# Performance work log

Measured on AMD Instinct MI355X. Metric: run time of the kernel, lower is better.

The kernel has to match this reference:

```python
import jax, jax.numpy as jnp
import numpy as np

IC, OC, ID, OD = 1152, 10, 8, 16   # input_caps, output_caps, input_dim, output_dim
N_ITER = 5
THRESHOLD = 1e-05
EPS = 1e-20


def setup_inputs() -> dict:
    key = jax.random.key(0)
    k1, k2 = jax.random.split(key)
    x = jax.random.uniform(k1, (32, IC, ID), dtype=jnp.float32)
    # replicate CapsLayer.__init__ + norm_weights(): uniform(0,1), normalize over
    # output_caps dim, clamp to threshold, renormalize
    w = jax.random.uniform(k2, (IC, OC, ID, OD), dtype=jnp.float32)
    w = w / (w.sum(axis=1, keepdims=True) + EPS)
    w = jnp.clip(w, THRESHOLD, None)
    w = w / (w.sum(axis=1, keepdims=True) + EPS)
    return {"x": x, "weights": w}


def nnmf_sbs(inp, weights):
    # inp: [B, ic, id], weights: [ic, oc, id, od] -> out: [B, ic, oc, od]
    B = inp.shape[0]
    out0 = jnp.full((B, IC, OC, OD), 1.0 / OD, dtype=inp.dtype)

    def body(out, _):
        h_w = out[:, :, :, None, :] * weights[None]          # [B,ic,oc,id,od]
        h_w = h_w / (h_w.sum(-1, keepdims=True) + EPS)       # normalize over od
        h_w = (h_w * inp[:, :, None, :, None]).sum(-2)       # reduce id -> [B,ic,oc,od]
        out = h_w / (h_w.sum(-1, keepdims=True) + EPS)       # normalize over od
        return out, None

    out, _ = jax.lax.scan(body, out0, None, length=N_ITER)
    return out


def reference(x, weights):
    x = x / (x.sum(-1, keepdims=True) + EPS)                 # normalize over input_dim
    h = nnmf_sbs(x, weights)                                 # [B,ic,oc,od]
    # reconstruct = (h.unsqueeze(-2) * weights).sum(-1) -> [B,ic,oc,id]
    reconstruct = jnp.einsum('bicd,iced->bice', h, weights)
    alpha = jnp.einsum('bice,bie->bic', reconstruct, x)      # [B,ic,oc]
    alpha = alpha / (alpha.sum(-1, keepdims=True) + EPS)     # normalize over oc
    return jnp.einsum('bicd,bic->bcd', h, alpha)             # sum over ic -> [B,oc,od]
```

## Files before the change

### kernel.cpp

```cpp
#include <hip/hip_runtime.h>

#define B_   32
#define ICN  1152
#define OCN  10
#define IDN  8
#define ODN  16
#define ODH  8
#define NIT  5
#define EPS  1e-20f
#define OUTN (B_ * OCN * ODN)
#define BGRP 11
#define NWAVE (BGRP * ICN)
#define WPB  4
#define NBLK (NWAVE / WPB)

__device__ __forceinline__ float dpp_swap1(float x) {
  return __int_as_float(__builtin_amdgcn_update_dpp(
      0, __float_as_int(x), 0xB1, 0xF, 0xF, true));
}

__global__ __launch_bounds__(256, 4) void caps_main(
    const float* __restrict__ xg, const float* __restrict__ wg,
    float* __restrict__ ws, float* __restrict__ outg, int atomic_out) {
  const int l = threadIdx.x & 63;
  const int wid = blockIdx.x * WPB + (threadIdx.x >> 6);
  const int ic = wid % ICN;
  const int bgrp = wid / ICN;
  const int grp = l / 20;
  const int q = l % 20;
  const int oc = q >> 1;
  const int half = q & 1;
  const int b = bgrp * 3 + grp;
  const bool valid = (grp < 3) && (b < B_);
  const int bb = (b < B_) ? b : (B_ - 1);

  float wr[IDN][ODH];
  {
    const float* wp = wg + ((size_t)ic * OCN + oc) * (IDN * ODN) + half * ODH;
#pragma unroll
    for (int id = 0; id < IDN; ++id) {
      const float4 v0 = *(const float4*)(wp + id * ODN);
      const float4 v1 = *(const float4*)(wp + id * ODN + 4);
      wr[id][0] = v0.x; wr[id][1] = v0.y; wr[id][2] = v0.z; wr[id][3] = v0.w;
      wr[id][4] = v1.x; wr[id][5] = v1.y; wr[id][6] = v1.z; wr[id][7] = v1.w;
    }
  }

  float xn[IDN];
  {
    const float* xp = xg + ((size_t)bb * ICN + ic) * IDN;
    const float4 a0 = ((const float4*)xp)[0];
    const float4 a1 = ((const float4*)xp)[1];
    xn[0] = a0.x; xn[1] = a0.y; xn[2] = a0.z; xn[3] = a0.w;
    xn[4] = a1.x; xn[5] = a1.y; xn[6] = a1.z; xn[7] = a1.w;
    const float s = ((xn[0] + xn[1]) + (xn[2] + xn[3])) +
                    ((xn[4] + xn[5]) + (xn[6] + xn[7]));
    const float r = __builtin_amdgcn_rcpf(s + EPS);
#pragma unroll
    for (int i = 0; i < IDN; ++i) xn[i] *= r;
  }

  float h[ODH];
#pragma unroll
  for (int k = 0; k < ODH; ++k) h[k] = 1.0f / ODN;

  for (int it = 0; it < NIT; ++it) {
    float pd[IDN];
#pragma unroll
    for (int id = 0; id < IDN; ++id) {
      float p = 0.f;
#pragma unroll
      for (int k = 0; k < ODH; ++k) p = fmaf(h[k], wr[id][k], p);
      pd[id] = p;
    }
    float tc[IDN];
#pragma unroll
    for (int id = 0; id < IDN; ++id) {
      const float den = pd[id] + dpp_swap1(pd[id]);
      tc[id] = xn[id] * __builtin_amdgcn_rcpf(den + EPS);
    }
    float hacc[ODH];
#pragma unroll
    for (int k = 0; k < ODH; ++k) hacc[k] = wr[0][k] * tc[0];
#pragma unroll
    for (int id = 1; id < IDN; ++id)
#pragma unroll
      for (int k = 0; k < ODH; ++k) hacc[k] = fmaf(wr[id][k], tc[id], hacc[k]);
#pragma unroll
    for (int k = 0; k < ODH; ++k) h[k] *= hacc[k];
    const float ps = ((h[0] + h[1]) + (h[2] + h[3])) +
                     ((h[4] + h[5]) + (h[6] + h[7]));
    const float hs = ps + dpp_swap1(ps);
    const float r = __builtin_amdgcn_rcpf(hs + EPS);
#pragma unroll
    for (int k = 0; k < ODH; ++k) h[k] *= r;
  }

  float ap = 0.f;
#pragma unroll
  for (int id = 0; id < IDN; ++id) {
    float rec = 0.f;
#pragma unroll
    for (int k = 0; k < ODH; ++k) rec = fmaf(h[k], wr[id][k], rec);
    ap = fmaf(rec, xn[id], ap);
  }
  const float af = ap + dpp_swap1(ap);
  float asum = 0.f;
  const int gbase = grp * 20;
#pragma unroll
  for (int k = 0; k < OCN; ++k) asum += __shfl(af, gbase + 2 * k, 64);
  const float an = af * __builtin_amdgcn_rcpf(asum + EPS);

  float o[ODH];
#pragma unroll
  for (int k = 0; k < ODH; ++k) o[k] = h[k] * an;

  if (valid) {
    if (!atomic_out) {
      float* dst = ws + (size_t)ic * OUTN + (bb * OCN + oc) * ODN + half * ODH;
      float4 v0, v1;
      v0.x = o[0]; v0.y = o[1]; v0.z = o[2]; v0.w = o[3];
      v1.x = o[4]; v1.y = o[5]; v1.z = o[6]; v1.w = o[7];
      ((float4*)dst)[0] = v0;
      ((float4*)dst)[1] = v1;
    } else {
      const int base = (bb * OCN + oc) * ODN + half * ODH;
#pragma unroll
      for (int k = 0; k < ODH; ++k) atomicAdd(outg + base + k, o[k]);
    }
  }
}

#define RSPLIT 32
#define RROWS  (ICN / RSPLIT)
__global__ void caps_reduce(const float* __restrict__ ws, float* __restrict__ outg) {
  const int j = blockIdx.x * 256 + threadIdx.x;
  const int r0 = blockIdx.y * RROWS;
  float s = 0.f;
#pragma unroll
  for (int r = 0; r < RROWS; ++r) s += ws[(size_t)(r0 + r) * OUTN + j];
  atomicAdd(outg + j, s);
}

extern "C" void kernel_launch(void* const* d_in, const int* in_sizes, int n_in,
                              void* d_out, int out_size, void* d_ws, size_t ws_size,
                              hipStream_t stream) {
  const float* x = (const float*)d_in[0];
  const float* w = (const float*)d_in[1];
  float* out = (float*)d_out;
  float* ws = (float*)d_ws;

  hipMemsetAsync(out, 0, OUTN * sizeof(float), stream);

  const size_t need = (size_t)ICN * OUTN * sizeof(float);

  if (ws_size >= need) {
    caps_main<<<NBLK, 256, 0, stream>>>(x, w, ws, out, 0);
    caps_reduce<<<dim3(OUTN / 256, RSPLIT), 256, 0, stream>>>(ws, out);
  } else {
    caps_main<<<NWAVE, 64, 0, stream>>>(x, w, nullptr, out, 1);
  }
}
```

Before: 92.51 us.

## Fuse cross-capsule reduction into main kernel via LDS and atomics

Removes the per-capsule workspace write and the separate reduction kernel. Each block now has 8 waves covering consecutive input capsules. They sum partial outputs in shared memory, and the block then issues one atomic add per output element. This avoids writing and re-reading the large workspace and saves a kernel launch. In exchange it relies on global atomics with ~144 contending adds per output address. The larger block with the same launch-bounds occupancy hint may also tighten the register budget.

```diff
diff --git a/kernel.cpp b/kernel.cpp
--- a/kernel.cpp
+++ b/kernel.cpp
@@ -11,7 +11,7 @@
 #define OUTN (B_ * OCN * ODN)
 #define BGRP 11
 #define NWAVE (BGRP * ICN)
-#define WPB  4
+#define WPB  8
 #define NBLK (NWAVE / WPB)
 
 __device__ __forceinline__ float dpp_swap1(float x) {
@@ -19,11 +19,13 @@
       0, __float_as_int(x), 0xB1, 0xF, 0xF, true));
 }
 
-__global__ __launch_bounds__(256, 4) void caps_main(
+__global__ __launch_bounds__(512, 4) void caps_main(
     const float* __restrict__ xg, const float* __restrict__ wg,
-    float* __restrict__ ws, float* __restrict__ outg, int atomic_out) {
+    float* __restrict__ outg) {
+  __shared__ float red[WPB * 512];
   const int l = threadIdx.x & 63;
-  const int wid = blockIdx.x * WPB + (threadIdx.x >> 6);
+  const int w = threadIdx.x >> 6;
+  const int wid = blockIdx.x * WPB + w;
   const int ic = wid % ICN;
   const int bgrp = wid / ICN;
   const int grp = l / 20;
@@ -31,7 +33,6 @@
   const int oc = q >> 1;
   const int half = q & 1;
   const int b = bgrp * 3 + grp;
-  const bool valid = (grp < 3) && (b < B_);
   const int bb = (b < B_) ? b : (B_ - 1);
 
   float wr[IDN][ODH];
@@ -111,35 +112,27 @@
   for (int k = 0; k < OCN; ++k) asum += __shfl(af, gbase + 2 * k, 64);
   const float an = af * __builtin_amdgcn_rcpf(asum + EPS);
 
-  float o[ODH];
 #pragma unroll
-  for (int k = 0; k < ODH; ++k) o[k] = h[k] * an;
+  for (int k = 0; k < ODH; ++k)
+    red[w * 512 + k * 64 + l] = h[k] * an;
 
-  if (valid) {
-    if (!atomic_out) {
-      float* dst = ws + (size_t)ic * OUTN + (bb * OCN + oc) * ODN + half * ODH;
-      float4 v0, v1;
-      v0.x = o[0]; v0.y = o[1]; v0.z = o[2]; v0.w = o[3];
-      v1.x = o[4]; v1.y = o[5]; v1.z = o[6]; v1.w = o[7];
-      ((float4*)dst)[0] = v0;
-      ((float4*)dst)[1] = v1;
-    } else {
-      const int base = (bb * OCN + oc) * ODN + half * ODH;
+  __syncthreads();
+
+  {
+    const int k2 = threadIdx.x >> 6;
+    const int l2 = threadIdx.x & 63;
+    const int grp2 = l2 / 20;
+    const int q2 = l2 % 20;
+    const int oc2 = q2 >> 1;
+    const int half2 = q2 & 1;
+    const int b2 = bgrp * 3 + grp2;
+    float s = 0.f;
 #pragma unroll
-      for (int k = 0; k < ODH; ++k) atomicAdd(outg + base + k, o[k]);
-    }
+    for (int ww = 0; ww < WPB; ++ww)
+      s += red[ww * 512 + k2 * 64 + l2];
+    if (grp2 < 3 && b2 < B_)
+      atomicAdd(outg + (b2 * OCN + oc2) * ODN + half2 * ODH + k2, s);
   }
-}
-
-#define RSPLIT 32
-#define RROWS  (ICN / RSPLIT)
-__global__ void caps_reduce(const float* __restrict__ ws, float* __restrict__ outg) {
-  const int j = blockIdx.x * 256 + threadIdx.x;
-  const int r0 = blockIdx.y * RROWS;
-  float s = 0.f;
-#pragma unroll
-  for (int r = 0; r < RROWS; ++r) s += ws[(size_t)(r0 + r) * OUTN + j];
-  atomicAdd(outg + j, s);
 }
 
 extern "C" void kernel_launch(void* const* d_in, const int* in_sizes, int n_in,
@@ -148,16 +141,8 @@
   const float* x = (const float*)d_in[0];
   const float* w = (const float*)d_in[1];
   float* out = (float*)d_out;
-  float* ws = (float*)d_ws;
+  (void)d_ws; (void)ws_size;
 
   hipMemsetAsync(out, 0, OUTN * sizeof(float), stream);
-
-  const size_t need = (size_t)ICN * OUTN * sizeof(float);
-
-  if (ws_size >= need) {
-    caps_main<<<NBLK, 256, 0, stream>>>(x, w, ws, out, 0);
-    caps_reduce<<<dim3(OUTN / 256, RSPLIT), 256, 0, stream>>>(ws, out);
-  } else {
-    caps_main<<<NWAVE, 64, 0, stream>>>(x, w, nullptr, out, 1);
-  }
+  caps_main<<<NBLK, 512, 0, stream>>>(x, w, out);
 }
```

After: 131.0 us. +41.6%, slower.
